# Kernel tuning notes

Measured on AMD Instinct MI355X. Metric: run time of the kernel, lower is better.

## Reference

```python
import jax, jax.numpy as jnp
import numpy as np
from jax import lax

N_SECTIONS, N_CHANNELS = 8, 128
KT, KF = 32, 16                 # kernel (time, freq)
LPOST = 400                     # section_length_postsyn
LPRE = KT + LPOST - 1           # 431, section_length_presyn
SECTION_DISTANCE = 400          # LPRE - overlap (overlap = 31)
N_TIMESTEPS, FREQ = 3231, 256
THRESHOLD = 15.0


def setup_inputs() -> dict:
    key = jax.random.key(0)
    k1, k2 = jax.random.split(key)
    # scale so mean conv response ~ threshold (512 taps * 0.8 * mean(X))
    X = jax.random.uniform(k1, (N_TIMESTEPS, FREQ), dtype=jnp.float32) * 0.073
    # SpykeTorch Convolution init: N(0.8, 0.05)
    W = 0.8 + 0.05 * jax.random.normal(k2, (N_SECTIONS, N_CHANNELS, 1, KT, KF), dtype=jnp.float32)
    return {"X": X, "W": W}


def _sections(X):
    # [S, LPRE, FREQ] overlapping time windows
    starts = jnp.arange(N_SECTIONS) * SECTION_DISTANCE
    idx = starts[:, None] + jnp.arange(LPRE)
    return X[idx]


def _conv_sections(X, W):
    Xs = _sections(X)  # [S, LPRE, FREQ]
    def conv1(xs, w):
        # xs: [LPRE, FREQ], w: [C, 1, KT, KF] -> [C, LPOST, FOUT]
        return lax.conv_general_dilated(xs[None, None], w, (1, 1), 'VALID')[0]
    return jax.vmap(conv1)(Xs, W)  # [S, C, LPOST, FOUT]


def reference(X, W):
    pots = _conv_sections(X, W)                              # [S, C, 400, 241]
    # sf.fire: zero potentials < threshold, then sign -> binary spikes
    spikes = (pots >= THRESHOLD).astype(pots.dtype)
    # Pooling((LPOST, KF)): max-pool, stride = window, no padding
    pool = lax.reduce_window(spikes, -jnp.inf, lax.max,
                             (1, 1, LPOST, KF), (1, 1, LPOST, KF), 'VALID')  # [S, C, 1, 15]
    # sf.get_k_winners(pool): dim 0 (sections) acts as the time dimension
    T = pool.shape[0]
    spk = jnp.sign(pool)
    earliest = jnp.clip((T - spk.sum(axis=0)).astype(jnp.int32), 0, T - 1)   # [C,1,Fp]
    values = jnp.take_along_axis(pool, earliest[None], axis=0)[0]            # earliest spike value
    trunc = spk * values[None]
    v = trunc.max() * T
    trunc = trunc + spk * v
    total = trunc.sum(axis=0)                                # [C, 1, Fp]
    max_val = total.max()
    # winners[0][0] = feature (channel) index of the flat argmax
    feat = jnp.argmax(total.reshape(-1)) // (total.shape[1] * total.shape[2])
    return jnp.where(max_val != 0, feat, -1).astype(jnp.int32)
```

## Files before the change

kernel.cpp:

```cpp
#include <hip/hip_runtime.h>


using int2v  = __attribute__((ext_vector_type(2))) int;
using int4v  = __attribute__((ext_vector_type(4))) int;
using int8v  = __attribute__((ext_vector_type(8))) int;
using f32x8  = __attribute__((ext_vector_type(8))) float;
using f32x16 = __attribute__((ext_vector_type(16))) float;

#define SCALE_ONE 0x7F7F7F7F
#define THRESH_Q  4920.0f

#if __has_builtin(__builtin_amdgcn_cvt_scalef32_pk_fp4_f32)
#define HWFP4 1
#else
#define HWFP4 0
#endif

__device__ __forceinline__ unsigned f4enc(float v) {
  float r2 = __builtin_rintf(v + v);
  float r1 = __builtin_rintf(v);
  return (v <= 2.f) ? (unsigned)r2
       : (v <= 4.f) ? (unsigned)r1 + 2u
       : (v < 5.f)  ? 6u : 7u;
}

__device__ __forceinline__ unsigned pack8(f32x8 v) {
  unsigned d = 0;
#if HWFP4
  d = __builtin_amdgcn_cvt_scalef32_pk_fp4_f32(d, v[0], v[1], 1.0f, 0);
  d = __builtin_amdgcn_cvt_scalef32_pk_fp4_f32(d, v[2], v[3], 1.0f, 1);
  d = __builtin_amdgcn_cvt_scalef32_pk_fp4_f32(d, v[4], v[5], 1.0f, 2);
  d = __builtin_amdgcn_cvt_scalef32_pk_fp4_f32(d, v[6], v[7], 1.0f, 3);
#else
#pragma unroll
  for (int e = 0; e < 8; ++e) d |= f4enc(v[e]) << (4 * e);
#endif
  return d;
}

__global__ __launch_bounds__(256) void prep_kernel(const float* __restrict__ W,
                                                   unsigned char* __restrict__ Wp4,
                                                   unsigned* __restrict__ pool) {
  int t = blockIdx.x * 256 + threadIdx.x;
  if (t < 1024) pool[t] = 0;
  int s = t >> 11, r = t & 2047, c = r >> 4, b = r & 15;
  const float* src = W + ((s * 128 + c) * 512 + b * 32);
  int4v o;
#pragma unroll
  for (int i = 0; i < 4; ++i) {
    f32x8 sv;
#pragma unroll
    for (int e = 0; e < 8; ++e) sv[e] = fmaxf(src[i * 8 + e], 0.f) * 4.f;
    o[i] = (int)pack8(sv);
  }
  *(int4v*)(Wp4 + s * 32768 + (b >> 1) * 4096 + (b & 1) * 2048 + c * 16) = o;
}

__global__ __launch_bounds__(512, 2) void conv_pool_kernel(const float* __restrict__ X,
                                                           const unsigned char* __restrict__ Wp4,
                                                           unsigned* __restrict__ pool) {
  __shared__ __align__(16) unsigned char Ash[2][8 * 512];
  __shared__ unsigned poolbits[2][32];
  __shared__ unsigned poolmask[128];

  const int tid = threadIdx.x;
  const int s   = blockIdx.x & 7;
  const int lb  = blockIdx.x >> 3;
  const int NT  = (lb < 6) ? 13 : 12;

  const int ok  = tid < 504;
  const int it0 = ok ? tid : 0;
  const int d0  = it0 / 63, r0 = it0 % 63;
  const float* Xs = X + (s * 400 + r0) * 256 + d0;

  const int w = tid >> 6, l = tid & 63;
  const int m31 = l & 31, ko = l >> 5;
  const int aoff = w * 512 + m31 * 8 + ko * 16;

  if (tid < 64) poolbits[tid >> 5][tid & 31] = 0;
  if (tid < 128) poolmask[tid] = 0;

  f32x8 xa, xb;
  {
    int tau = lb, tt = tau / 30, ft = tau % 30;
    int t0 = (tt == 12) ? 368 : tt * 32;
    const float* xp = Xs + t0 * 256 + ft * 8;
#pragma unroll
    for (int e = 0; e < 8; ++e) { xa[e] = xp[e]; xb[e] = xp[e + 8]; }
  }
  __builtin_amdgcn_sched_barrier(0);

  int4v Breg[8][4];
  {
    const unsigned char* wb = Wp4 + s * 32768 + ko * 2048 + m31 * 16;
#pragma unroll
    for (int ch = 0; ch < 8; ++ch)
#pragma unroll
      for (int nt = 0; nt < 4; ++nt)
        Breg[ch][nt] = *(const int4v*)(wb + ch * 4096 + nt * 512);
  }

  xa *= 82.f; xb *= 82.f;
  if (ok) *(int2v*)&Ash[0][d0 * 512 + r0 * 8] = (int2v){(int)pack8(xa), (int)pack8(xb)};
  if (NT > 1) {
    int tau = lb + 32, tt = tau / 30, ft = tau % 30;
    int t0 = (tt == 12) ? 368 : tt * 32;
    const float* xp = Xs + t0 * 256 + ft * 8;
#pragma unroll
    for (int e = 0; e < 8; ++e) { xa[e] = xp[e]; xb[e] = xp[e + 8]; }
  }
  __syncthreads();

#pragma unroll 1
  for (int i = 0; i < NT; ++i) {
    const unsigned char* ab = &Ash[i & 1][0];

    f32x16 acc[4];
#pragma unroll
    for (int b = 0; b < 4; ++b)
#pragma unroll
      for (int e = 0; e < 16; ++e) acc[b][e] = 0.f;
#pragma unroll
    for (int ch = 0; ch < 8; ++ch) {
      int2v alo = *(const int2v*)&ab[aoff + ch * 32];
      int2v ahi = *(const int2v*)&ab[aoff + ch * 32 + 8];
      int8v Af = {alo[0], alo[1], ahi[0], ahi[1], 0, 0, 0, 0};
#pragma unroll
      for (int nt = 0; nt < 4; ++nt) {
        int8v Bf = {Breg[ch][nt][0], Breg[ch][nt][1],
                    Breg[ch][nt][2], Breg[ch][nt][3], 0, 0, 0, 0};
        acc[nt] = __builtin_amdgcn_mfma_scale_f32_32x32x64_f8f6f4(
            Af, Bf, acc[nt], 4, 4, 0, SCALE_ONE, 0, SCALE_ONE);
      }
    }

    unsigned sp = 0;
#pragma unroll
    for (int nt = 0; nt < 4; ++nt) {
      float m0 = -1e30f;
#pragma unroll
      for (int e = 0; e < 16; ++e) m0 = fmaxf(m0, acc[nt][e]);
      if (m0 >= THRESH_Q) sp |= (1u << nt);
    }
    sp |= __shfl_xor(sp, 32, 64);
    if (l < 32 && sp) atomicOr(&poolbits[i & 1][m31], sp);

    if (i + 1 < NT) {
      xa *= 82.f; xb *= 82.f;
      if (ok)
        *(int2v*)&Ash[(i + 1) & 1][d0 * 512 + r0 * 8] =
            (int2v){(int)pack8(xa), (int)pack8(xb)};
      if (i + 2 < NT) {
        int tau = lb + 32 * (i + 2), tt = tau / 30, ft = tau % 30;
        int t0 = (tt == 12) ? 368 : tt * 32;
        const float* xp = Xs + t0 * 256 + ft * 8;
#pragma unroll
        for (int e = 0; e < 8; ++e) { xa[e] = xp[e]; xb[e] = xp[e + 8]; }
      }
    }

    __syncthreads();

    if (tid < 32) {
      unsigned bits = poolbits[i & 1][tid];
      poolbits[i & 1][tid] = 0;
      if (bits) {
        int fp = ((lb + 32 * i) % 30) >> 1;
        unsigned bit = 1u << fp;
#pragma unroll
        for (int nt = 0; nt < 4; ++nt)
          if ((bits >> nt) & 1) poolmask[nt * 32 + tid] |= bit;
      }
    }
  }

  __syncthreads();
  if (tid < 128) {
    unsigned m = poolmask[tid];
    if (m) atomicOr(&pool[s * 128 + tid], m);
  }
}

__global__ __launch_bounds__(256) void winner_kernel(const unsigned* __restrict__ pool,
                                                     float* __restrict__ out) {
  __shared__ unsigned pb[1024];
  __shared__ int bestpk;
  int tid = threadIdx.x;
  if (tid == 0) bestpk = 0;
  for (int q = tid; q < 1024; q += 256) pb[q] = pool[q];
  __syncthreads();

  int lbest = 0;
  for (int p = tid; p < 1920; p += 256) {
    int c = p / 15, f = p % 15;
    int cnt = 0;
#pragma unroll
    for (int s2 = 0; s2 < 8; ++s2) cnt += (pb[s2 * 128 + c] >> f) & 1;
    if (cnt > 0) {
      int early = 8 - cnt;
      int val = (pb[early * 128 + c] >> f) & 1;
      int total = cnt * (8 + val);
      int pack = (total << 12) | (4095 - p);
      if (pack > lbest) lbest = pack;
    }
  }
  atomicMax(&bestpk, lbest);
  __syncthreads();
  if (tid == 0) {
    int feat = (4095 - (bestpk & 4095)) / 15;
    out[0] = (bestpk != 0) ? (float)feat : -1.0f;
  }
}

extern "C" void kernel_launch(void* const* d_in, const int* in_sizes, int n_in,
                              void* d_out, int out_size, void* d_ws, size_t ws_size,
                              hipStream_t stream) {
  (void)in_sizes; (void)n_in; (void)out_size; (void)ws_size;
  const float* X = (const float*)d_in[0];
  const float* W = (const float*)d_in[1];
  unsigned char* Wp4 = (unsigned char*)d_ws;
  unsigned* pool = (unsigned*)((char*)d_ws + (1 << 18));

  prep_kernel<<<64, 256, 0, stream>>>(W, Wp4, pool);
  conv_pool_kernel<<<256, 512, 0, stream>>>(X, Wp4, pool);
  winner_kernel<<<1, 256, 0, stream>>>(pool, (float*)d_out);
}
```

Before: 84.84 us.

## Make LDS tiles wave-private and drop per-iteration block barriers

Each wave now loads and packs exactly the FP4 activation slice it later reads from LDS, so the per-iteration __syncthreads and shared poolbits exchange are no longer needed. Pool spike bits are accumulated in per-lane registers across iterations and merged into shared poolmask once at the end. This removes block-wide barriers and LDS atomics from the main loop. The cost is a different global load pattern for X and reliance on intra-wave LDS ordering.

```diff
diff --git a/kernel.cpp b/kernel.cpp
--- a/kernel.cpp
+++ b/kernel.cpp
@@ -60,7 +60,6 @@
                                                            const unsigned char* __restrict__ Wp4,
                                                            unsigned* __restrict__ pool) {
   __shared__ __align__(16) unsigned char Ash[2][8 * 512];
-  __shared__ unsigned poolbits[2][32];
   __shared__ unsigned poolmask[128];
 
   const int tid = threadIdx.x;
@@ -68,25 +67,30 @@
   const int lb  = blockIdx.x >> 3;
   const int NT  = (lb < 6) ? 13 : 12;
 
-  const int ok  = tid < 504;
-  const int it0 = ok ? tid : 0;
-  const int d0  = it0 / 63, r0 = it0 % 63;
-  const float* Xs = X + (s * 400 + r0) * 256 + d0;
-
   const int w = tid >> 6, l = tid & 63;
   const int m31 = l & 31, ko = l >> 5;
+
+  if (tid < 128) poolmask[tid] = 0;
+  __syncthreads();
+
+  const int rA  = l >> 1, hA = l & 1;
+  const int okB = l < 62;
+  const int rB  = okB ? 32 + (l >> 1) : 62;
+  const int col = w + hA * 8;
+  const int sA  = w * 512 + rA * 8 + hA * 4;
+  const int sB  = w * 512 + (32 + (l >> 1)) * 8 + hA * 4;
+  const float* Xrow = X + (s * 400) * 256 + col;
+
   const int aoff = w * 512 + m31 * 8 + ko * 16;
-
-  if (tid < 64) poolbits[tid >> 5][tid & 31] = 0;
-  if (tid < 128) poolmask[tid] = 0;
 
   f32x8 xa, xb;
   {
     int tau = lb, tt = tau / 30, ft = tau % 30;
     int t0 = (tt == 12) ? 368 : tt * 32;
-    const float* xp = Xs + t0 * 256 + ft * 8;
-#pragma unroll
-    for (int e = 0; e < 8; ++e) { xa[e] = xp[e]; xb[e] = xp[e + 8]; }
+    const float* pa = Xrow + (t0 + rA) * 256 + ft * 8;
+    const float* pb = Xrow + (t0 + rB) * 256 + ft * 8;
+#pragma unroll
+    for (int e = 0; e < 8; ++e) { xa[e] = pa[e]; xb[e] = pb[e]; }
   }
   __builtin_amdgcn_sched_barrier(0);
 
@@ -100,20 +104,36 @@
         Breg[ch][nt] = *(const int4v*)(wb + ch * 4096 + nt * 512);
   }
 
-  xa *= 82.f; xb *= 82.f;
-  if (ok) *(int2v*)&Ash[0][d0 * 512 + r0 * 8] = (int2v){(int)pack8(xa), (int)pack8(xb)};
+  *(unsigned*)&Ash[0][sA] = pack8(xa * 82.f);
+  if (okB) *(unsigned*)&Ash[0][sB] = pack8(xb * 82.f);
   if (NT > 1) {
     int tau = lb + 32, tt = tau / 30, ft = tau % 30;
     int t0 = (tt == 12) ? 368 : tt * 32;
-    const float* xp = Xs + t0 * 256 + ft * 8;
-#pragma unroll
-    for (int e = 0; e < 8; ++e) { xa[e] = xp[e]; xb[e] = xp[e + 8]; }
-  }
-  __syncthreads();
+    const float* pa = Xrow + (t0 + rA) * 256 + ft * 8;
+    const float* pb = Xrow + (t0 + rB) * 256 + ft * 8;
+#pragma unroll
+    for (int e = 0; e < 8; ++e) { xa[e] = pa[e]; xb[e] = pb[e]; }
+  }
+
+  unsigned pm[4] = {0, 0, 0, 0};
 
 #pragma unroll 1
   for (int i = 0; i < NT; ++i) {
-    const unsigned char* ab = &Ash[i & 1][0];
+    const unsigned char* rb = &Ash[i & 1][0];
+    unsigned char* wbuf = &Ash[(i + 1) & 1][0];
+
+    if (i + 1 < NT) {
+      *(unsigned*)&wbuf[sA] = pack8(xa * 82.f);
+      if (okB) *(unsigned*)&wbuf[sB] = pack8(xb * 82.f);
+    }
+    if (i + 2 < NT) {
+      int tau = lb + 32 * (i + 2), tt = tau / 30, ft = tau % 30;
+      int t0 = (tt == 12) ? 368 : tt * 32;
+      const float* pa = Xrow + (t0 + rA) * 256 + ft * 8;
+      const float* pb = Xrow + (t0 + rB) * 256 + ft * 8;
+#pragma unroll
+      for (int e = 0; e < 8; ++e) { xa[e] = pa[e]; xb[e] = pb[e]; }
+    }
 
     f32x16 acc[4];
 #pragma unroll
@@ -122,8 +142,8 @@
       for (int e = 0; e < 16; ++e) acc[b][e] = 0.f;
 #pragma unroll
     for (int ch = 0; ch < 8; ++ch) {
-      int2v alo = *(const int2v*)&ab[aoff + ch * 32];
-      int2v ahi = *(const int2v*)&ab[aoff + ch * 32 + 8];
+      int2v alo = *(const int2v*)&rb[aoff + ch * 32];
+      int2v ahi = *(const int2v*)&rb[aoff + ch * 32 + 8];
       int8v Af = {alo[0], alo[1], ahi[0], ahi[1], 0, 0, 0, 0};
 #pragma unroll
       for (int nt = 0; nt < 4; ++nt) {
@@ -143,37 +163,19 @@
       if (m0 >= THRESH_Q) sp |= (1u << nt);
     }
     sp |= __shfl_xor(sp, 32, 64);
-    if (l < 32 && sp) atomicOr(&poolbits[i & 1][m31], sp);
-
-    if (i + 1 < NT) {
-      xa *= 82.f; xb *= 82.f;
-      if (ok)
-        *(int2v*)&Ash[(i + 1) & 1][d0 * 512 + r0 * 8] =
-            (int2v){(int)pack8(xa), (int)pack8(xb)};
-      if (i + 2 < NT) {
-        int tau = lb + 32 * (i + 2), tt = tau / 30, ft = tau % 30;
-        int t0 = (tt == 12) ? 368 : tt * 32;
-        const float* xp = Xs + t0 * 256 + ft * 8;
-#pragma unroll
-        for (int e = 0; e < 8; ++e) { xa[e] = xp[e]; xb[e] = xp[e + 8]; }
-      }
-    }
-
-    __syncthreads();
-
-    if (tid < 32) {
-      unsigned bits = poolbits[i & 1][tid];
-      poolbits[i & 1][tid] = 0;
-      if (bits) {
-        int fp = ((lb + 32 * i) % 30) >> 1;
-        unsigned bit = 1u << fp;
-#pragma unroll
-        for (int nt = 0; nt < 4; ++nt)
-          if ((bits >> nt) & 1) poolmask[nt * 32 + tid] |= bit;
-      }
-    }
-  }
-
+    {
+      int fp = ((lb + 32 * i) % 30) >> 1;
+#pragma unroll
+      for (int nt = 0; nt < 4; ++nt)
+        pm[nt] |= ((sp >> nt) & 1u) << fp;
+    }
+  }
+
+  if (l < 32) {
+#pragma unroll
+    for (int nt = 0; nt < 4; ++nt)
+      if (pm[nt]) atomicOr(&poolmask[nt * 32 + m31], pm[nt]);
+  }
   __syncthreads();
   if (tid < 128) {
     unsigned m = poolmask[tid];
```

New measurement: 83.83 us (median of 2 runs). Within noise of the previous version (-1.2%).
